# Kernel tuning notes

Measured on AMD Instinct MI355X. Metric: run time of the kernel, lower is better.

## Reference

```python
import math
import jax, jax.numpy as jnp
import numpy as np

N, E = 20000, 640000
S_DIM, Z_DIM, H, QK, VD = 64, 64, 4, 8, 8
EPS = 1e-8


def quat_rotate(v, q):
    # v: [..., 3], q: [..., 4] (w, x, y, z), broadcastable. Unit-quaternion rotation:
    # v' = v + 2*(w*(u x v) + u x (u x v))
    w = q[..., 0:1]
    u = q[..., 1:4]
    uv = jnp.cross(u, v)
    return v + 2.0 * (w * uv + jnp.cross(u, uv))


def setup_inputs() -> dict:
    key = jax.random.key(0)
    ks = jax.random.split(key, 16)
    s = jax.random.normal(ks[0], (N, S_DIM), dtype=jnp.float32)
    z = jax.random.normal(ks[1], (E, Z_DIM), dtype=jnp.float32)
    edge_index = jax.random.randint(ks[2], (2, E), 0, N)
    quaternion = jax.random.normal(ks[3], (N, 4), dtype=jnp.float32)
    quaternion = quaternion / jnp.linalg.norm(quaternion, axis=-1, keepdims=True)
    translation = jax.random.normal(ks[4], (N, 3), dtype=jnp.float32)
    sc_s = 1.0 / math.sqrt(S_DIM)
    sc_z = 1.0 / math.sqrt(Z_DIM)
    # weights stored [in, out] so y = x @ W (equivalent to torch x @ W.T)
    Wq_s = jax.random.normal(ks[5], (S_DIM, H * S_DIM), dtype=jnp.float32) * sc_s
    Wk_s = jax.random.normal(ks[6], (S_DIM, H * S_DIM), dtype=jnp.float32) * sc_s
    Wv_s = jax.random.normal(ks[7], (S_DIM, H * S_DIM), dtype=jnp.float32) * sc_s
    Wq_v = jax.random.normal(ks[8], (S_DIM, H * QK * 3), dtype=jnp.float32) * sc_s
    Wk_v = jax.random.normal(ks[9], (S_DIM, H * QK * 3), dtype=jnp.float32) * sc_s
    Wv_v = jax.random.normal(ks[10], (S_DIM, H * VD * 3), dtype=jnp.float32) * sc_s
    Wb = jax.random.normal(ks[11], (Z_DIM, H), dtype=jnp.float32) * sc_z
    bb = jnp.zeros((H,), dtype=jnp.float32)
    Wdz = jax.random.normal(ks[12], (Z_DIM, Z_DIM // 4), dtype=jnp.float32) * sc_z
    bdz = jnp.zeros((Z_DIM // 4,), dtype=jnp.float32)
    head_weights = jnp.full((H,), 0.541324854612918, dtype=jnp.float32)  # softplus^{-1}(1)
    concat_dim = Z_DIM // 4 + S_DIM + VD * 4
    Wout = jax.random.normal(ks[13], (H * concat_dim, S_DIM), dtype=jnp.float32) / math.sqrt(H * concat_dim)
    bout = jnp.zeros((S_DIM,), dtype=jnp.float32)
    return {
        's': s, 'z': z, 'edge_index': edge_index, 'quaternion': quaternion,
        'translation': translation, 'Wq_s': Wq_s, 'Wk_s': Wk_s, 'Wv_s': Wv_s,
        'Wq_v': Wq_v, 'Wk_v': Wk_v, 'Wv_v': Wv_v, 'Wb': Wb, 'bb': bb,
        'Wdz': Wdz, 'bdz': bdz, 'head_weights': head_weights,
        'Wout': Wout, 'bout': bout,
    }


def reference(s, z, edge_index, quaternion, translation,
              Wq_s, Wk_s, Wv_s, Wq_v, Wk_v, Wv_v,
              Wb, bb, Wdz, bdz, head_weights, Wout, bout):
    idx_i, idx_j = edge_index[0], edge_index[1]
    n = s.shape[0]
    h = head_weights.shape[0]
    qk = Wq_v.shape[1] // (3 * h)
    vd = Wv_v.shape[1] // (3 * h)

    q_scalar = (s @ Wq_s).reshape(n, h, -1)
    k_scalar = (s @ Wk_s).reshape(n, h, -1)
    v_scalar = (s @ Wv_s).reshape(n, h, -1)

    def to_points(x):
        # torch.split into 3 chunks then stack(dim=-1): [n, 3*c] -> [n, c, 3]
        c = x.shape[-1] // 3
        return jnp.swapaxes(x.reshape(n, 3, c), 1, 2)

    quat_b = quaternion[:, None, :]
    trans_b = translation[:, None, :]
    q_vec = (quat_rotate(to_points(s @ Wq_v), quat_b) + trans_b).reshape(n, h, qk, 3)
    k_vec = (quat_rotate(to_points(s @ Wk_v), quat_b) + trans_b).reshape(n, h, qk, 3)
    v_vec = (quat_rotate(to_points(s @ Wv_v), quat_b) + trans_b).reshape(n, h, vd, 3)

    b_bias = z @ Wb + bb  # [E, H]

    attn = jnp.sum(k_scalar[idx_i] * q_scalar[idx_j], axis=-1)  # [E, H]
    attn = attn * math.sqrt(1.0 / 3 * qk) + math.sqrt(1.0 / 3) * b_bias

    disp = q_vec[idx_i] - k_vec[idx_j]            # [E, H, qk, 3]
    vec_att = jnp.sum(disp * disp, axis=-1)       # [E, H, qk]
    hw = jax.nn.softplus(head_weights)[None, :, None]
    vec_att = jnp.sum(vec_att * hw, axis=-1) * math.sqrt(1.0 / (3 * (qk * 9.0 / 2))) * (-0.5)
    attn = attn + vec_att

    # segment softmax over destination node idx_i
    seg_max = jax.ops.segment_max(attn, idx_i, num_segments=n)
    ea = jnp.exp(attn - seg_max[idx_i])
    denom = jax.ops.segment_sum(ea, idx_i, num_segments=n)
    attn = ea / denom[idx_i]                      # [E, H]

    out_scalar = jax.ops.segment_sum(attn[:, :, None] * v_scalar[idx_i], idx_i, num_segments=n)
    out_scalar = out_scalar.reshape(n, -1)

    out_vec = jax.ops.segment_sum(attn[:, :, None, None] * v_vec[idx_i], idx_i, num_segments=n)
    out_vec = out_vec - translation[:, None, None, :]
    q_conj = jnp.concatenate([quaternion[:, :1], -quaternion[:, 1:]], axis=-1)
    out_vec = quat_rotate(out_vec, q_conj[:, None, None, :])   # [n, h, vd, 3]
    out_vec_norm = jnp.sqrt(jnp.sum(out_vec * out_vec, axis=-1) + EPS).reshape(n, -1)
    out_vec_flat = out_vec.reshape(n, -1, 3)

    pair_z = z @ Wdz + bdz                         # [E, z/4]
    out_pair = jax.ops.segment_sum(attn[:, :, None] * pair_z[:, None, :], idx_i, num_segments=n)
    out_pair = out_pair.reshape(n, -1)

    feats = jnp.concatenate([out_scalar,
                             out_vec_flat[..., 0], out_vec_flat[..., 1], out_vec_flat[..., 2],
                             out_vec_norm, out_pair], axis=-1)
    return feats @ Wout + bout
```

## Files before the change

### kernel.cpp

```cpp
#include <hip/hip_runtime.h>
#include <stdint.h>


#define C_SQRT83  1.6329931618554518f
#define C_SQRT13  0.5773502691896258f
#define C_VEC    -0.04811252243246881f

__device__ __forceinline__ unsigned short f2bf(float f){
  unsigned u = __float_as_uint(f);
  u += 0x7fffu + ((u >> 16) & 1u);
  return (unsigned short)(u >> 16);
}
__device__ __forceinline__ unsigned pack2(float a, float b){
  return (unsigned)f2bf(a) | ((unsigned)f2bf(b) << 16);
}
__device__ __forceinline__ float bflo(unsigned u){ return __uint_as_float(u << 16); }
__device__ __forceinline__ float bfhi(unsigned u){ return __uint_as_float(u & 0xffff0000u); }

__device__ __forceinline__ void quat_rot(float w, float ux, float uy, float uz,
                                         float vx, float vy, float vz,
                                         float& ox, float& oy, float& oz){
  float cx = uy*vz - uz*vy;
  float cy = uz*vx - ux*vz;
  float cz = ux*vy - uy*vx;
  float dx = uy*cz - uz*cy;
  float dy = uz*cx - ux*cz;
  float dz = ux*cy - uy*cx;
  ox = vx + 2.f*(w*cx + dx);
  oy = vy + 2.f*(w*cy + dy);
  oz = vz + 2.f*(w*cz + dz);
}


__global__ __launch_bounds__(256) void k_count(const int* __restrict__ ei,
                                               unsigned* __restrict__ counts,
                                               unsigned* __restrict__ rank, int ne){
  int e = blockIdx.x*256 + threadIdx.x;
  if (e >= ne) return;
  rank[e] = atomicAdd(&counts[ei[e]], 1u);
}

__global__ __launch_bounds__(256) void k_scan(const unsigned* __restrict__ counts,
                                              unsigned* __restrict__ row_off, int n){
  __shared__ unsigned part[256];
  int t = threadIdx.x;
  int chunk = (n + 255) >> 8;
  int s0 = t*chunk, s1 = min(s0 + chunk, n);
  unsigned sum = 0;
  for (int k = s0; k < s1; ++k) sum += counts[k];
  part[t] = sum; __syncthreads();
  for (int off = 1; off < 256; off <<= 1){
    unsigned v = (t >= off) ? part[t-off] : 0u;
    __syncthreads();
    part[t] += v;
    __syncthreads();
  }
  unsigned run = (t == 0) ? 0u : part[t-1];
  for (int k = s0; k < s1; ++k){
    row_off[k] = run; run += counts[k];
  }
  if (t == 255) row_off[n] = part[255];
}


#define BN 32

__device__ __forceinline__ void pass256(const float* __restrict__ W,
                                        const float stT[64][40], int cg, int sl,
                                        float acc[8][4]){
  #pragma unroll
  for (int i=0;i<8;i++){ acc[i][0]=0.f; acc[i][1]=0.f; acc[i][2]=0.f; acc[i][3]=0.f; }
  #pragma unroll 4
  for (int k = 0; k < 64; ++k){
    const float4 w  = *(const float4*)(W + (size_t)k*256 + cg*4);
    const float4 n0 = *(const float4*)&stT[k][sl*8];
    const float4 n1 = *(const float4*)&stT[k][sl*8+4];
    acc[0][0]+=n0.x*w.x; acc[0][1]+=n0.x*w.y; acc[0][2]+=n0.x*w.z; acc[0][3]+=n0.x*w.w;
    acc[1][0]+=n0.y*w.x; acc[1][1]+=n0.y*w.y; acc[1][2]+=n0.y*w.z; acc[1][3]+=n0.y*w.w;
    acc[2][0]+=n0.z*w.x; acc[2][1]+=n0.z*w.y; acc[2][2]+=n0.z*w.z; acc[2][3]+=n0.z*w.w;
    acc[3][0]+=n0.w*w.x; acc[3][1]+=n0.w*w.y; acc[3][2]+=n0.w*w.z; acc[3][3]+=n0.w*w.w;
    acc[4][0]+=n1.x*w.x; acc[4][1]+=n1.x*w.y; acc[4][2]+=n1.x*w.z; acc[4][3]+=n1.x*w.w;
    acc[5][0]+=n1.y*w.x; acc[5][1]+=n1.y*w.y; acc[5][2]+=n1.y*w.z; acc[5][3]+=n1.y*w.w;
    acc[6][0]+=n1.z*w.x; acc[6][1]+=n1.z*w.y; acc[6][2]+=n1.z*w.z; acc[6][3]+=n1.z*w.w;
    acc[7][0]+=n1.w*w.x; acc[7][1]+=n1.w*w.y; acc[7][2]+=n1.w*w.z; acc[7][3]+=n1.w*w.w;
  }
}

__device__ __forceinline__ void pass96(const float* __restrict__ W,
                                       const float stT[64][40], int cgp, int slp,
                                       float acc[4][4]){
  #pragma unroll
  for (int i=0;i<4;i++){ acc[i][0]=0.f; acc[i][1]=0.f; acc[i][2]=0.f; acc[i][3]=0.f; }
  if (cgp >= 24) return;
  #pragma unroll 4
  for (int k = 0; k < 64; ++k){
    const float4 w = *(const float4*)(W + (size_t)k*96 + cgp*4);
    const float4 nv = *(const float4*)&stT[k][slp*4];
    acc[0][0]+=nv.x*w.x; acc[0][1]+=nv.x*w.y; acc[0][2]+=nv.x*w.z; acc[0][3]+=nv.x*w.w;
    acc[1][0]+=nv.y*w.x; acc[1][1]+=nv.y*w.y; acc[1][2]+=nv.y*w.z; acc[1][3]+=nv.y*w.w;
    acc[2][0]+=nv.z*w.x; acc[2][1]+=nv.z*w.y; acc[2][2]+=nv.z*w.z; acc[2][3]+=nv.z*w.w;
    acc[3][0]+=nv.w*w.x; acc[3][1]+=nv.w*w.y; acc[3][2]+=nv.w*w.z; acc[3][3]+=nv.w*w.w;
  }
}

__global__ __launch_bounds__(256) void k_proj(
    const float* __restrict__ s, const float* __restrict__ quat, const float* __restrict__ trans,
    const float* __restrict__ Wqs, const float* __restrict__ Wks, const float* __restrict__ Wvs,
    const float* __restrict__ Wqv, const float* __restrict__ Wkv, const float* __restrict__ Wvv,
    unsigned* __restrict__ qs, unsigned* __restrict__ ks, float* __restrict__ vs,
    unsigned* __restrict__ qv, unsigned* __restrict__ kv, float* __restrict__ vv, int n)
{
  __shared__ float stT[64][40];
  __shared__ float pt[BN][97];
  const int tid = threadIdx.x;
  const int node0 = blockIdx.x * BN;

  #pragma unroll
  for (int r = 0; r < 2; ++r){
    const int idx = tid + r*256;
    const int nd = idx >> 4, c4 = idx & 15;
    const int g = node0 + nd;
    float4 v = make_float4(0.f,0.f,0.f,0.f);
    if (g < n) v = *(const float4*)(s + (size_t)g*64 + c4*4);
    stT[c4*4+0][nd]=v.x; stT[c4*4+1][nd]=v.y; stT[c4*4+2][nd]=v.z; stT[c4*4+3][nd]=v.w;
  }
  __syncthreads();

  const int cg = tid & 63, sl = tid >> 6;
  const int cgp = tid & 31, slp = tid >> 5;
  float acc[8][4];

  pass256(Wqs, stT, cg, sl, acc);
  #pragma unroll
  for (int i=0;i<8;i++){
    const int g = node0 + sl*8 + i;
    if (g < n){
      uint2 u; u.x = pack2(acc[i][0],acc[i][1]); u.y = pack2(acc[i][2],acc[i][3]);
      *(uint2*)(qs + (size_t)g*128 + cg*2) = u;
    }
  }
  pass256(Wks, stT, cg, sl, acc);
  #pragma unroll
  for (int i=0;i<8;i++){
    const int g = node0 + sl*8 + i;
    if (g < n){
      uint2 u; u.x = pack2(acc[i][0],acc[i][1]); u.y = pack2(acc[i][2],acc[i][3]);
      *(uint2*)(ks + (size_t)g*128 + cg*2) = u;
    }
  }
  pass256(Wvs, stT, cg, sl, acc);
  #pragma unroll
  for (int i=0;i<8;i++){
    const int g = node0 + sl*8 + i;
    if (g < n){
      float4 f; f.x=acc[i][0]; f.y=acc[i][1]; f.z=acc[i][2]; f.w=acc[i][3];
      *(float4*)(vs + (size_t)g*256 + cg*4) = f;
    }
  }

  float pac[4][4];

  pass96(Wqv, stT, cgp, slp, pac);
  __syncthreads();
  if (cgp < 24){
    #pragma unroll
    for (int i=0;i<4;i++){
      #pragma unroll
      for (int c=0;c<4;c++) pt[slp*4+i][cgp*4+c] = pac[i][c];
    }
  }
  __syncthreads();
  #pragma unroll
  for (int r = 0; r < 2; ++r){
    const int t2 = tid + r*256;
    const int nd = t2 >> 4, pp = t2 & 15;
    const int g = node0 + nd;
    if (g < n){
      const float4 q4 = *(const float4*)(quat + (size_t)g*4);
      const float tx = trans[(size_t)g*3], ty = trans[(size_t)g*3+1], tz = trans[(size_t)g*3+2];
      float x0,y0,z0,x1,y1,z1;
      quat_rot(q4.x,q4.y,q4.z,q4.w, pt[nd][2*pp],   pt[nd][32+2*pp],   pt[nd][64+2*pp],   x0,y0,z0);
      quat_rot(q4.x,q4.y,q4.z,q4.w, pt[nd][2*pp+1], pt[nd][32+2*pp+1], pt[nd][64+2*pp+1], x1,y1,z1);
      x0+=tx; y0+=ty; z0+=tz; x1+=tx; y1+=ty; z1+=tz;
      unsigned* d = qv + (size_t)g*48 + pp*3;
      d[0] = pack2(x0,y0); d[1] = pack2(z0,x1); d[2] = pack2(y1,z1);
    }
  }

  pass96(Wkv, stT, cgp, slp, pac);
  __syncthreads();
  if (cgp < 24){
    #pragma unroll
    for (int i=0;i<4;i++){
      #pragma unroll
      for (int c=0;c<4;c++) pt[slp*4+i][cgp*4+c] = pac[i][c];
    }
  }
  __syncthreads();
  #pragma unroll
  for (int r = 0; r < 2; ++r){
    const int t2 = tid + r*256;
    const int nd = t2 >> 4, pp = t2 & 15;
    const int g = node0 + nd;
    if (g < n){
      const float4 q4 = *(const float4*)(quat + (size_t)g*4);
      const float tx = trans[(size_t)g*3], ty = trans[(size_t)g*3+1], tz = trans[(size_t)g*3+2];
      float x0,y0,z0,x1,y1,z1;
      quat_rot(q4.x,q4.y,q4.z,q4.w, pt[nd][2*pp],   pt[nd][32+2*pp],   pt[nd][64+2*pp],   x0,y0,z0);
      quat_rot(q4.x,q4.y,q4.z,q4.w, pt[nd][2*pp+1], pt[nd][32+2*pp+1], pt[nd][64+2*pp+1], x1,y1,z1);
      x0+=tx; y0+=ty; z0+=tz; x1+=tx; y1+=ty; z1+=tz;
      unsigned* d = kv + (size_t)g*48 + pp*3;
      d[0] = pack2(x0,y0); d[1] = pack2(z0,x1); d[2] = pack2(y1,z1);
    }
  }

  pass96(Wvv, stT, cgp, slp, pac);
  __syncthreads();
  if (cgp < 24){
    #pragma unroll
    for (int i=0;i<4;i++){
      #pragma unroll
      for (int c=0;c<4;c++) pt[slp*4+i][cgp*4+c] = pac[i][c];
    }
  }
  __syncthreads();
  #pragma unroll
  for (int r = 0; r < 12; ++r){
    const int idx = tid + r*256;
    const int nd = idx / 96, col = idx - nd*96;
    const int g = node0 + nd;
    if (g < n) vv[(size_t)g*96 + col] = pt[nd][col];
  }
}


__global__ __launch_bounds__(256) void k_zf(
    const int* __restrict__ ei, const unsigned* __restrict__ rank,
    const unsigned* __restrict__ roff, const float* __restrict__ z,
    const float* __restrict__ Wb,  const float* __restrict__ bb,
    const float* __restrict__ Wdz, const float* __restrict__ bdz,
    unsigned* __restrict__ rec, int ne)
{
  __shared__ float zT[16][258];
  const int tid = threadIdx.x;
  const int E0  = blockIdx.x * 256;
  const int e   = E0 + tid;
  const bool full = (E0 + 256 <= ne);

  int i = 0, j = 0; unsigned pos = 0;
  if (e < ne){
    i = ei[e]; j = ei[ne + e];
    pos = roff[i] + rank[e];
  }

  float b4[4] = {0.f,0.f,0.f,0.f};
  float pacc[16];
  #pragma unroll
  for (int c=0;c<16;c++) pacc[c]=0.f;

  if (full){
    #pragma unroll
    for (int c = 0; c < 4; ++c){
      if (c) __syncthreads();
      #pragma unroll
      for (int q = 0; q < 4; ++q){
        const int idx = tid + q*256;
        const int row = idx >> 2, f4 = idx & 3;
        const float4 v = *(const float4*)(z + (size_t)(E0+row)*64 + c*16 + f4*4);
        zT[f4*4+0][row]=v.x; zT[f4*4+1][row]=v.y;
        zT[f4*4+2][row]=v.z; zT[f4*4+3][row]=v.w;
      }
      __syncthreads();
      const int kb = c*16;
      #pragma unroll
      for (int kk = 0; kk < 16; ++kk){
        const float zk = zT[kk][tid];
        const int k = kb + kk;
        const float4 wb = *(const float4*)(Wb + k*4);
        b4[0]+=zk*wb.x; b4[1]+=zk*wb.y; b4[2]+=zk*wb.z; b4[3]+=zk*wb.w;
        const float* wd = Wdz + k*16;
        const float4 w0=*(const float4*)(wd),   w1=*(const float4*)(wd+4),
                     w2=*(const float4*)(wd+8), w3=*(const float4*)(wd+12);
        pacc[ 0]+=zk*w0.x; pacc[ 1]+=zk*w0.y; pacc[ 2]+=zk*w0.z; pacc[ 3]+=zk*w0.w;
        pacc[ 4]+=zk*w1.x; pacc[ 5]+=zk*w1.y; pacc[ 6]+=zk*w1.z; pacc[ 7]+=zk*w1.w;
        pacc[ 8]+=zk*w2.x; pacc[ 9]+=zk*w2.y; pacc[10]+=zk*w2.z; pacc[11]+=zk*w2.w;
        pacc[12]+=zk*w3.x; pacc[13]+=zk*w3.y; pacc[14]+=zk*w3.z; pacc[15]+=zk*w3.w;
      }
    }
  } else if (e < ne){
    const float* zr = z + (size_t)e*64;
    for (int k4 = 0; k4 < 16; ++k4){
      const float4 zv = *(const float4*)(zr + 4*k4);
      #pragma unroll
      for (int kk = 0; kk < 4; ++kk){
        const int k = 4*k4 + kk;
        const float zk = (kk==0)?zv.x:((kk==1)?zv.y:((kk==2)?zv.z:zv.w));
        const float4 wb = *(const float4*)(Wb + k*4);
        b4[0]+=zk*wb.x; b4[1]+=zk*wb.y; b4[2]+=zk*wb.z; b4[3]+=zk*wb.w;
        const float* wd = Wdz + k*16;
        const float4 w0=*(const float4*)(wd),   w1=*(const float4*)(wd+4),
                     w2=*(const float4*)(wd+8), w3=*(const float4*)(wd+12);
        pacc[ 0]+=zk*w0.x; pacc[ 1]+=zk*w0.y; pacc[ 2]+=zk*w0.z; pacc[ 3]+=zk*w0.w;
        pacc[ 4]+=zk*w1.x; pacc[ 5]+=zk*w1.y; pacc[ 6]+=zk*w1.z; pacc[ 7]+=zk*w1.w;
        pacc[ 8]+=zk*w2.x; pacc[ 9]+=zk*w2.y; pacc[10]+=zk*w2.z; pacc[11]+=zk*w2.w;
        pacc[12]+=zk*w3.x; pacc[13]+=zk*w3.y; pacc[14]+=zk*w3.z; pacc[15]+=zk*w3.w;
      }
    }
  }

  if (e < ne){
    #pragma unroll
    for (int c=0;c<16;c++) pacc[c] += bdz[c];
    uint4 u0, u1;
    u0.x=pack2(pacc[0],pacc[1]);   u0.y=pack2(pacc[2],pacc[3]);
    u0.z=pack2(pacc[4],pacc[5]);   u0.w=pack2(pacc[6],pacc[7]);
    u1.x=pack2(pacc[8],pacc[9]);   u1.y=pack2(pacc[10],pacc[11]);
    u1.z=pack2(pacc[12],pacc[13]); u1.w=pack2(pacc[14],pacc[15]);
    float4 bo;
    bo.x = C_SQRT13*(b4[0] + bb[0]);
    bo.y = C_SQRT13*(b4[1] + bb[1]);
    bo.z = C_SQRT13*(b4[2] + bb[2]);
    bo.w = C_SQRT13*(b4[3] + bb[3]);
    uint4* d = (uint4*)rec + (size_t)pos*4;
    d[0] = *(uint4*)&bo;
    d[1] = u0;
    d[2] = u1;
    d[3] = make_uint4((unsigned)i, (unsigned)j, 0u, 0u);
  }
}


__global__ __launch_bounds__(256) void k_edge(
    const float* __restrict__ hwts,
    const unsigned* __restrict__ qs, const unsigned* __restrict__ ks,
    const unsigned* __restrict__ qv, const unsigned* __restrict__ kv,
    unsigned* __restrict__ rec, int ne)
{
  const int tid = threadIdx.x;
  const int P0  = blockIdx.x * 256;
  const int p   = P0 + tid;
  const bool full = (P0 + 256 <= ne);

  const float hw0 = C_VEC * log1pf(__expf(hwts[0]));
  const float hw1 = C_VEC * log1pf(__expf(hwts[1]));
  const float hw2 = C_VEC * log1pf(__expf(hwts[2]));
  const float hw3 = C_VEC * log1pf(__expf(hwts[3]));

  int i = 0, j = 0;
  float4 bias = make_float4(0.f,0.f,0.f,0.f);
  if (p < ne){
    bias = *(const float4*)((const float*)rec + (size_t)p*16);
    const uint2 ij = *(const uint2*)(rec + (size_t)p*16 + 12);
    i = (int)ij.x; j = (int)ij.y;
  }

  if (full){
    const int l = tid & 63;
    const int c = l & 3, g = l >> 2;
    #pragma unroll
    for (int sb = 0; sb < 4; ++sb){
      const int el = sb*16 + g;
      const int ie = __shfl(i, el, 64);
      const int je = __shfl(j, el, 64);

      const uint4* kr = (const uint4*)ks + (size_t)ie*32;
      const uint4* qr = (const uint4*)qs + (size_t)je*32;
      float s0=0.f, s1=0.f, s2=0.f, s3=0.f;
      #pragma unroll
      for (int it = 0; it < 8; ++it){
        const uint4 a = kr[it*4 + c];
        const uint4 b = qr[it*4 + c];
        float d;
        d  = bflo(a.x)*bflo(b.x) + bfhi(a.x)*bfhi(b.x);
        d += bflo(a.y)*bflo(b.y) + bfhi(a.y)*bfhi(b.y);
        d += bflo(a.z)*bflo(b.z) + bfhi(a.z)*bfhi(b.z);
        d += bflo(a.w)*bflo(b.w) + bfhi(a.w)*bfhi(b.w);
        if      (it < 2) s0 += d;
        else if (it < 4) s1 += d;
        else if (it < 6) s2 += d;
        else             s3 += d;
      }

      const uint4* qvr = (const uint4*)qv + (size_t)ie*12;
      const uint4* kvr = (const uint4*)kv + (size_t)je*12;
      float v0=0.f, v1=0.f, v2=0.f, v3=0.f;
      {
        const uint4 a = qvr[c], b = kvr[c];
        float d, t;
        t = bflo(a.x)-bflo(b.x); d  = t*t;  t = bfhi(a.x)-bfhi(b.x); d += t*t;
        t = bflo(a.y)-bflo(b.y); d += t*t;  t = bfhi(a.y)-bfhi(b.y); d += t*t;
        t = bflo(a.z)-bflo(b.z); d += t*t;  t = bfhi(a.z)-bfhi(b.z); d += t*t;
        t = bflo(a.w)-bflo(b.w); d += t*t;  t = bfhi(a.w)-bfhi(b.w); d += t*t;
        if (c < 3) v0 += d; else v1 += d;
      }
      {
        const uint4 a = qvr[4+c], b = kvr[4+c];
        float d, t;
        t = bflo(a.x)-bflo(b.x); d  = t*t;  t = bfhi(a.x)-bfhi(b.x); d += t*t;
        t = bflo(a.y)-bflo(b.y); d += t*t;  t = bfhi(a.y)-bfhi(b.y); d += t*t;
        t = bflo(a.z)-bflo(b.z); d += t*t;  t = bfhi(a.z)-bfhi(b.z); d += t*t;
        t = bflo(a.w)-bflo(b.w); d += t*t;  t = bfhi(a.w)-bfhi(b.w); d += t*t;
        if (c < 2) v1 += d; else v2 += d;
      }
      {
        const uint4 a = qvr[8+c], b = kvr[8+c];
        float d, t;
        t = bflo(a.x)-bflo(b.x); d  = t*t;  t = bfhi(a.x)-bfhi(b.x); d += t*t;
        t = bflo(a.y)-bflo(b.y); d += t*t;  t = bfhi(a.y)-bfhi(b.y); d += t*t;
        t = bflo(a.z)-bflo(b.z); d += t*t;  t = bfhi(a.z)-bfhi(b.z); d += t*t;
        t = bflo(a.w)-bflo(b.w); d += t*t;  t = bfhi(a.w)-bfhi(b.w); d += t*t;
        if (c < 1) v2 += d; else v3 += d;
      }

      float p0 = C_SQRT83*s0 + hw0*v0;
      float p1 = C_SQRT83*s1 + hw1*v1;
      float p2 = C_SQRT83*s2 + hw2*v2;
      float p3 = C_SQRT83*s3 + hw3*v3;
      #pragma unroll
      for (int msk = 1; msk < 4; msk <<= 1){
        p0 += __shfl_xor(p0, msk, 64);
        p1 += __shfl_xor(p1, msk, 64);
        p2 += __shfl_xor(p2, msk, 64);
        p3 += __shfl_xor(p3, msk, 64);
      }
      const float pc = (c==0)?p0:((c==1)?p1:((c==2)?p2:p3));

      const int srcbase = (l & 15) << 2;
      const float q0 = __shfl(pc, srcbase+0, 64);
      const float q1 = __shfl(pc, srcbase+1, 64);
      const float q2 = __shfl(pc, srcbase+2, 64);
      const float q3 = __shfl(pc, srcbase+3, 64);
      if ((l >> 4) == sb){
        float4 lg; lg.x = q0 + bias.x; lg.y = q1 + bias.y;
        lg.z = q2 + bias.z; lg.w = q3 + bias.w;
        *((uint4*)rec + (size_t)p*4) = *(uint4*)&lg;
      }
    }
  } else if (p < ne){
    const uint4* kr = (const uint4*)ks + (size_t)i*32;
    const uint4* qr = (const uint4*)qs + (size_t)j*32;
    float sdot[4];
    #pragma unroll
    for (int h = 0; h < 4; ++h){
      float acc = 0.f;
      #pragma unroll
      for (int cc = 0; cc < 8; ++cc){
        const uint4 a = kr[h*8+cc];
        const uint4 b = qr[h*8+cc];
        acc += bflo(a.x)*bflo(b.x) + bfhi(a.x)*bfhi(b.x);
        acc += bflo(a.y)*bflo(b.y) + bfhi(a.y)*bfhi(b.y);
        acc += bflo(a.z)*bflo(b.z) + bfhi(a.z)*bfhi(b.z);
        acc += bflo(a.w)*bflo(b.w) + bfhi(a.w)*bfhi(b.w);
      }
      sdot[h] = acc;
    }
    const uint4* qvr = (const uint4*)qv + (size_t)i*12;
    const uint4* kvr = (const uint4*)kv + (size_t)j*12;
    float vsum[4];
    #pragma unroll
    for (int h = 0; h < 4; ++h){
      float acc = 0.f;
      #pragma unroll
      for (int cc = 0; cc < 3; ++cc){
        const uint4 a = qvr[h*3+cc];
        const uint4 b = kvr[h*3+cc];
        float d;
        d = bflo(a.x)-bflo(b.x); acc += d*d;  d = bfhi(a.x)-bfhi(b.x); acc += d*d;
        d = bflo(a.y)-bflo(b.y); acc += d*d;  d = bfhi(a.y)-bfhi(b.y); acc += d*d;
        d = bflo(a.z)-bflo(b.z); acc += d*d;  d = bfhi(a.z)-bfhi(b.z); acc += d*d;
        d = bflo(a.w)-bflo(b.w); acc += d*d;  d = bfhi(a.w)-bfhi(b.w); acc += d*d;
      }
      vsum[h] = acc;
    }
    float4 lg;
    lg.x = C_SQRT83*sdot[0] + bias.x + hw0*vsum[0];
    lg.y = C_SQRT83*sdot[1] + bias.y + hw1*vsum[1];
    lg.z = C_SQRT83*sdot[2] + bias.z + hw2*vsum[2];
    lg.w = C_SQRT83*sdot[3] + bias.w + hw3*vsum[3];
    *((uint4*)rec + (size_t)p*4) = *(uint4*)&lg;
  }
}


__global__ __launch_bounds__(256) void k_soft(
    const unsigned* __restrict__ rec,
    const unsigned* __restrict__ row_off, float* __restrict__ out_pair, int n)
{
  const int node = blockIdx.x*4 + (threadIdx.x >> 6);
  if (node >= n) return;
  const int lane = threadIdx.x & 63;
  const int beg = (int)row_off[node], end = (int)row_off[node+1];
  const float* recf = (const float*)rec;

  float m[4] = {-3.0e38f,-3.0e38f,-3.0e38f,-3.0e38f};
  for (int p = beg + lane; p < end; p += 64){
    const float4 l = *(const float4*)(recf + (size_t)p*16);
    m[0]=fmaxf(m[0],l.x); m[1]=fmaxf(m[1],l.y); m[2]=fmaxf(m[2],l.z); m[3]=fmaxf(m[3],l.w);
  }
  #pragma unroll
  for (int msk = 1; msk < 64; msk <<= 1){
    #pragma unroll
    for (int h=0;h<4;h++) m[h] = fmaxf(m[h], __shfl_xor(m[h], msk));
  }
  float S[4] = {0.f,0.f,0.f,0.f};
  for (int p = beg + lane; p < end; p += 64){
    const float4 l = *(const float4*)(recf + (size_t)p*16);
    S[0]+=__expf(l.x-m[0]); S[1]+=__expf(l.y-m[1]);
    S[2]+=__expf(l.z-m[2]); S[3]+=__expf(l.w-m[3]);
  }
  #pragma unroll
  for (int msk = 1; msk < 64; msk <<= 1){
    #pragma unroll
    for (int h=0;h<4;h++) S[h] += __shfl_xor(S[h], msk);
  }
  float inv[4];
  #pragma unroll
  for (int h=0;h<4;h++) inv[h] = (S[h] > 0.f) ? (1.f/S[h]) : 0.f;

  const int e4 = lane >> 4, c = lane & 15;
  float acc[4] = {0.f,0.f,0.f,0.f};
  for (int base = beg; base < end; base += 4){
    const int p = base + e4;
    if (p < end){
      const float4 l = *(const float4*)(recf + (size_t)p*16);
      const unsigned u = rec[(size_t)p*16 + 4 + (c>>1)];
      const float pzv = (c & 1) ? bfhi(u) : bflo(u);
      acc[0] += __expf(l.x-m[0]) * pzv;
      acc[1] += __expf(l.y-m[1]) * pzv;
      acc[2] += __expf(l.z-m[2]) * pzv;
      acc[3] += __expf(l.w-m[3]) * pzv;
    }
  }
  #pragma unroll
  for (int msk = 16; msk < 64; msk <<= 1){
    #pragma unroll
    for (int h=0;h<4;h++) acc[h] += __shfl_xor(acc[h], msk);
  }
  const int hOut = lane >> 4;
  out_pair[(size_t)node*64 + lane] = acc[hOut] * inv[hOut];
}


__global__ __launch_bounds__(256) void k_out(
    const float* __restrict__ vs, const float* __restrict__ vv,
    const float* __restrict__ out_pair, const unsigned* __restrict__ row_off,
    const float* __restrict__ quat, const float* __restrict__ trans,
    const float* __restrict__ Wout, const float* __restrict__ bout,
    float* __restrict__ out, int n)
{
  __shared__ float feats[32][448];
  __shared__ int degs[32];
  const int tid = threadIdx.x;
  const int node0 = blockIdx.x*32;

  if (tid < 32){
    const int g = node0 + tid;
    degs[tid] = (g < n) ? (int)(row_off[g+1] - row_off[g]) : 1;
  }
  __syncthreads();

  for (int x = tid; x < 32*256; x += 256){
    const int nd = x >> 8, c = x & 255;
    const int g = node0 + nd;
    feats[nd][c] = (g < n && degs[nd] > 0) ? vs[(size_t)g*256 + c] : 0.f;
  }
  for (int x = tid; x < 32*64; x += 256){
    const int nd = x >> 6, c = x & 63;
    const int g = node0 + nd;
    feats[nd][384 + c] = (g < n) ? out_pair[(size_t)g*64 + c] : 0.f;
  }
  for (int x = tid; x < 32*32; x += 256){
    const int nd = x >> 5, pt = x & 31;
    const int g = node0 + nd;
    float X=0.f, Y=0.f, Z=0.f;
    if (g < n){
      if (degs[nd] > 0){
        X = vv[(size_t)g*96 + pt];
        Y = vv[(size_t)g*96 + 32 + pt];
        Z = vv[(size_t)g*96 + 64 + pt];
      } else {
        const float4 q4 = *(const float4*)(quat + (size_t)g*4);
        const float tx = trans[(size_t)g*3], ty = trans[(size_t)g*3+1], tz = trans[(size_t)g*3+2];
        quat_rot(q4.x, -q4.y, -q4.z, -q4.w, -tx, -ty, -tz, X, Y, Z);
      }
    }
    feats[nd][256 + pt] = X;
    feats[nd][288 + pt] = Y;
    feats[nd][320 + pt] = Z;
    feats[nd][352 + pt] = sqrtf(X*X + Y*Y + Z*Z + 1e-8f);
  }
  __syncthreads();

  const int lane = tid & 63;
  const int wave = tid >> 6;
  float acc[8];
  #pragma unroll
  for (int q8=0;q8<8;q8++) acc[q8]=0.f;

  for (int k0 = 0; k0 < 448; k0 += 4){
    const float w0 = Wout[(size_t)(k0+0)*64 + lane];
    const float w1 = Wout[(size_t)(k0+1)*64 + lane];
    const float w2 = Wout[(size_t)(k0+2)*64 + lane];
    const float w3 = Wout[(size_t)(k0+3)*64 + lane];
    #pragma unroll
    for (int q8 = 0; q8 < 8; ++q8){
      const float4 f = *(const float4*)&feats[wave*8 + q8][k0];
      acc[q8] += f.x*w0 + f.y*w1 + f.z*w2 + f.w*w3;
    }
  }
  const float bo = bout[lane];
  #pragma unroll
  for (int q8 = 0; q8 < 8; ++q8){
    const int g = node0 + wave*8 + q8;
    if (g < n) out[(size_t)g*64 + lane] = acc[q8] + bo;
  }
}


extern "C" void kernel_launch(void* const* d_in, const int* in_sizes, int n_in,
                              void* d_out, int out_size, void* d_ws, size_t ws_size,
                              hipStream_t stream) {
  const float* s     = (const float*)d_in[0];
  const float* z     = (const float*)d_in[1];
  const int*   ei    = (const int*)  d_in[2];
  const float* quat  = (const float*)d_in[3];
  const float* trans = (const float*)d_in[4];
  const float* Wqs   = (const float*)d_in[5];
  const float* Wks   = (const float*)d_in[6];
  const float* Wvs   = (const float*)d_in[7];
  const float* Wqv   = (const float*)d_in[8];
  const float* Wkv   = (const float*)d_in[9];
  const float* Wvv   = (const float*)d_in[10];
  const float* Wb    = (const float*)d_in[11];
  const float* bb    = (const float*)d_in[12];
  const float* Wdz   = (const float*)d_in[13];
  const float* bdz   = (const float*)d_in[14];
  const float* hwts  = (const float*)d_in[15];
  const float* Wout  = (const float*)d_in[16];
  const float* bout  = (const float*)d_in[17];
  float* out = (float*)d_out;

  const int n  = in_sizes[0] / 64;
  const int ne = in_sizes[1] / 64;

  size_t off = 0;
  char* base = (char*)d_ws;
  auto take = [&](size_t bytes)->char* {
    char* p = base + off;
    off += (bytes + 255) & ~(size_t)255;
    return p;
  };
  unsigned* qs     = (unsigned*)take((size_t)n*512);
  unsigned* ks     = (unsigned*)take((size_t)n*512);
  unsigned* qvt    = (unsigned*)take((size_t)n*192);
  unsigned* kvt    = (unsigned*)take((size_t)n*192);
  float*    vs     = (float*)   take((size_t)n*1024);
  float*    vv     = (float*)   take((size_t)n*384);
  unsigned* rec    = (unsigned*)take((size_t)ne*64);
  unsigned* counts = (unsigned*)take((size_t)n*4);
  unsigned* roff   = (unsigned*)take((size_t)(n+1)*4);
  unsigned* rank   = (unsigned*)take((size_t)ne*4);
  float*    opair  = (float*)   take((size_t)n*256);
  (void)ws_size; (void)n_in; (void)out_size;

  const int gbE = (ne + 255) / 256;

  hipMemsetAsync(counts, 0, (size_t)n*4, stream);
  k_count<<<gbE, 256, 0, stream>>>(ei, counts, rank, ne);
  k_scan <<<1,   256, 0, stream>>>(counts, roff, n);
  k_proj <<<(n + BN - 1)/BN, 256, 0, stream>>>(s, quat, trans, Wqs, Wks, Wvs, Wqv, Wkv, Wvv,
                                               qs, ks, vs, qvt, kvt, vv, n);
  k_zf   <<<gbE, 256, 0, stream>>>(ei, rank, roff, z, Wb, bb, Wdz, bdz, rec, ne);
  k_edge <<<gbE, 256, 0, stream>>>(hwts, qs, ks, qvt, kvt, rec, ne);
  k_soft <<<(n + 3)/4, 256, 0, stream>>>(rec, roff, opair, n);
  k_out  <<<(n + 31)/32, 256, 0, stream>>>(vs, vv, opair, roff, quat, trans,
                                           Wout, bout, out, n);
}
```

Baseline: 598.3 us.

## Split edge logits into separate array, prefetch z tiles, shrink output node tile

Moves the per-edge logits/bias out of the 64-byte edge record into a compact 16-byte-per-edge array. The softmax max/sum passes and the edge kernel then read dense float4s instead of strided records. The z-projection kernel now double-buffers its global loads in registers, so the next chunk loads while the current chunk computes. The output projection kernel uses 16 nodes per block instead of 32, which cuts shared memory and raises block count but gives less Wout reuse per block.

```diff
diff --git a/kernel.cpp b/kernel.cpp
--- a/kernel.cpp
+++ b/kernel.cpp
@@ -239,7 +239,7 @@
     const unsigned* __restrict__ roff, const float* __restrict__ z,
     const float* __restrict__ Wb,  const float* __restrict__ bb,
     const float* __restrict__ Wdz, const float* __restrict__ bdz,
-    unsigned* __restrict__ rec, int ne)
+    float* __restrict__ lg, unsigned* __restrict__ rec, int ne)
 {
   __shared__ float zT[16][258];
   const int tid = threadIdx.x;
@@ -259,18 +259,33 @@
   for (int c=0;c<16;c++) pacc[c]=0.f;
 
   if (full){
+    float4 rg[4];
+    #pragma unroll
+    for (int q = 0; q < 4; ++q){
+      const int idx = tid + q*256;
+      const int row = idx >> 2, f4 = idx & 3;
+      rg[q] = *(const float4*)(z + (size_t)(E0+row)*64 + f4*4);
+    }
+    #pragma unroll
+    for (int q = 0; q < 4; ++q){
+      const int idx = tid + q*256;
+      const int row = idx >> 2, f4 = idx & 3;
+      zT[f4*4+0][row]=rg[q].x; zT[f4*4+1][row]=rg[q].y;
+      zT[f4*4+2][row]=rg[q].z; zT[f4*4+3][row]=rg[q].w;
+    }
+    __syncthreads();
+
     #pragma unroll
     for (int c = 0; c < 4; ++c){
-      if (c) __syncthreads();
-      #pragma unroll
-      for (int q = 0; q < 4; ++q){
-        const int idx = tid + q*256;
-        const int row = idx >> 2, f4 = idx & 3;
-        const float4 v = *(const float4*)(z + (size_t)(E0+row)*64 + c*16 + f4*4);
-        zT[f4*4+0][row]=v.x; zT[f4*4+1][row]=v.y;
-        zT[f4*4+2][row]=v.z; zT[f4*4+3][row]=v.w;
-      }
-      __syncthreads();
+      float4 rn[4];
+      if (c < 3){
+        #pragma unroll
+        for (int q = 0; q < 4; ++q){
+          const int idx = tid + q*256;
+          const int row = idx >> 2, f4 = idx & 3;
+          rn[q] = *(const float4*)(z + (size_t)(E0+row)*64 + (c+1)*16 + f4*4);
+        }
+      }
       const int kb = c*16;
       #pragma unroll
       for (int kk = 0; kk < 16; ++kk){
@@ -286,6 +301,17 @@
         pacc[ 8]+=zk*w2.x; pacc[ 9]+=zk*w2.y; pacc[10]+=zk*w2.z; pacc[11]+=zk*w2.w;
         pacc[12]+=zk*w3.x; pacc[13]+=zk*w3.y; pacc[14]+=zk*w3.z; pacc[15]+=zk*w3.w;
       }
+      __syncthreads();
+      if (c < 3){
+        #pragma unroll
+        for (int q = 0; q < 4; ++q){
+          const int idx = tid + q*256;
+          const int row = idx >> 2, f4 = idx & 3;
+          zT[f4*4+0][row]=rn[q].x; zT[f4*4+1][row]=rn[q].y;
+          zT[f4*4+2][row]=rn[q].z; zT[f4*4+3][row]=rn[q].w;
+        }
+        __syncthreads();
+      }
     }
   } else if (e < ne){
     const float* zr = z + (size_t)e*64;
@@ -321,11 +347,11 @@
     bo.y = C_SQRT13*(b4[1] + bb[1]);
     bo.z = C_SQRT13*(b4[2] + bb[2]);
     bo.w = C_SQRT13*(b4[3] + bb[3]);
+    *((float4*)lg + pos) = bo;
     uint4* d = (uint4*)rec + (size_t)pos*4;
-    d[0] = *(uint4*)&bo;
-    d[1] = u0;
-    d[2] = u1;
-    d[3] = make_uint4((unsigned)i, (unsigned)j, 0u, 0u);
+    d[0] = u0;
+    d[1] = u1;
+    d[2] = make_uint4((unsigned)i, (unsigned)j, 0u, 0u);
   }
 }
 
@@ -334,7 +360,7 @@
     const float* __restrict__ hwts,
     const unsigned* __restrict__ qs, const unsigned* __restrict__ ks,
     const unsigned* __restrict__ qv, const unsigned* __restrict__ kv,
-    unsigned* __restrict__ rec, int ne)
+    const unsigned* __restrict__ rec, float* __restrict__ lg, int ne)
 {
   const int tid = threadIdx.x;
   const int P0  = blockIdx.x * 256;
@@ -349,8 +375,8 @@
   int i = 0, j = 0;
   float4 bias = make_float4(0.f,0.f,0.f,0.f);
   if (p < ne){
-    bias = *(const float4*)((const float*)rec + (size_t)p*16);
-    const uint2 ij = *(const uint2*)(rec + (size_t)p*16 + 12);
+    bias = *((const float4*)lg + p);
+    const uint2 ij = *(const uint2*)(rec + (size_t)p*16 + 8);
     i = (int)ij.x; j = (int)ij.y;
   }
 
@@ -431,9 +457,9 @@
       const float q2 = __shfl(pc, srcbase+2, 64);
       const float q3 = __shfl(pc, srcbase+3, 64);
       if ((l >> 4) == sb){
-        float4 lg; lg.x = q0 + bias.x; lg.y = q1 + bias.y;
-        lg.z = q2 + bias.z; lg.w = q3 + bias.w;
-        *((uint4*)rec + (size_t)p*4) = *(uint4*)&lg;
+        float4 lgv; lgv.x = q0 + bias.x; lgv.y = q1 + bias.y;
+        lgv.z = q2 + bias.z; lgv.w = q3 + bias.w;
+        *((float4*)lg + p) = lgv;
       }
     }
   } else if (p < ne){
@@ -472,29 +498,29 @@
       }
       vsum[h] = acc;
     }
-    float4 lg;
-    lg.x = C_SQRT83*sdot[0] + bias.x + hw0*vsum[0];
-    lg.y = C_SQRT83*sdot[1] + bias.y + hw1*vsum[1];
-    lg.z = C_SQRT83*sdot[2] + bias.z + hw2*vsum[2];
-    lg.w = C_SQRT83*sdot[3] + bias.w + hw3*vsum[3];
-    *((uint4*)rec + (size_t)p*4) = *(uint4*)&lg;
+    float4 lgv;
+    lgv.x = C_SQRT83*sdot[0] + bias.x + hw0*vsum[0];
+    lgv.y = C_SQRT83*sdot[1] + bias.y + hw1*vsum[1];
+    lgv.z = C_SQRT83*sdot[2] + bias.z + hw2*vsum[2];
+    lgv.w = C_SQRT83*sdot[3] + bias.w + hw3*vsum[3];
+    *((float4*)lg + p) = lgv;
   }
 }
 
 
 __global__ __launch_bounds__(256) void k_soft(
-    const unsigned* __restrict__ rec,
+    const float* __restrict__ lg, const unsigned* __restrict__ rec,
     const unsigned* __restrict__ row_off, float* __restrict__ out_pair, int n)
 {
   const int node = blockIdx.x*4 + (threadIdx.x >> 6);
   if (node >= n) return;
   const int lane = threadIdx.x & 63;
   const int beg = (int)row_off[node], end = (int)row_off[node+1];
-  const float* recf = (const float*)rec;
+  const float4* lg4 = (const float4*)lg;
 
   float m[4] = {-3.0e38f,-3.0e38f,-3.0e38f,-3.0e38f};
   for (int p = beg + lane; p < end; p += 64){
-    const float4 l = *(const float4*)(recf + (size_t)p*16);
+    const float4 l = lg4[p];
     m[0]=fmaxf(m[0],l.x); m[1]=fmaxf(m[1],l.y); m[2]=fmaxf(m[2],l.z); m[3]=fmaxf(m[3],l.w);
   }
   #pragma unroll
@@ -504,7 +530,7 @@
   }
   float S[4] = {0.f,0.f,0.f,0.f};
   for (int p = beg + lane; p < end; p += 64){
-    const float4 l = *(const float4*)(recf + (size_t)p*16);
+    const float4 l = lg4[p];
     S[0]+=__expf(l.x-m[0]); S[1]+=__expf(l.y-m[1]);
     S[2]+=__expf(l.z-m[2]); S[3]+=__expf(l.w-m[3]);
   }
@@ -522,8 +548,8 @@
   for (int base = beg; base < end; base += 4){
     const int p = base + e4;
     if (p < end){
-      const float4 l = *(const float4*)(recf + (size_t)p*16);
-      const unsigned u = rec[(size_t)p*16 + 4 + (c>>1)];
+      const float4 l = lg4[p];
+      const unsigned u = rec[(size_t)p*16 + (c>>1)];
       const float pzv = (c & 1) ? bfhi(u) : bflo(u);
       acc[0] += __expf(l.x-m[0]) * pzv;
       acc[1] += __expf(l.y-m[1]) * pzv;
@@ -540,6 +566,8 @@
   out_pair[(size_t)node*64 + lane] = acc[hOut] * inv[hOut];
 }
 
+
+#define BNO 16
 
 __global__ __launch_bounds__(256) void k_out(
     const float* __restrict__ vs, const float* __restrict__ vv,
@@ -548,28 +576,28 @@
     const float* __restrict__ Wout, const float* __restrict__ bout,
     float* __restrict__ out, int n)
 {
-  __shared__ float feats[32][448];
-  __shared__ int degs[32];
+  __shared__ float feats[BNO][448];
+  __shared__ int degs[BNO];
   const int tid = threadIdx.x;
-  const int node0 = blockIdx.x*32;
-
-  if (tid < 32){
+  const int node0 = blockIdx.x*BNO;
+
+  if (tid < BNO){
     const int g = node0 + tid;
     degs[tid] = (g < n) ? (int)(row_off[g+1] - row_off[g]) : 1;
   }
   __syncthreads();
 
-  for (int x = tid; x < 32*256; x += 256){
+  for (int x = tid; x < BNO*256; x += 256){
     const int nd = x >> 8, c = x & 255;
     const int g = node0 + nd;
     feats[nd][c] = (g < n && degs[nd] > 0) ? vs[(size_t)g*256 + c] : 0.f;
   }
-  for (int x = tid; x < 32*64; x += 256){
+  for (int x = tid; x < BNO*64; x += 256){
     const int nd = x >> 6, c = x & 63;
     const int g = node0 + nd;
     feats[nd][384 + c] = (g < n) ? out_pair[(size_t)g*64 + c] : 0.f;
   }
-  for (int x = tid; x < 32*32; x += 256){
+  for (int x = tid; x < BNO*32; x += 256){
     const int nd = x >> 5, pt = x & 31;
     const int g = node0 + nd;
     float X=0.f, Y=0.f, Z=0.f;
@@ -593,9 +621,9 @@
 
   const int lane = tid & 63;
   const int wave = tid >> 6;
-  float acc[8];
-  #pragma unroll
-  for (int q8=0;q8<8;q8++) acc[q8]=0.f;
+  float acc[4];
+  #pragma unroll
+  for (int q4=0;q4<4;q4++) acc[q4]=0.f;
 
   for (int k0 = 0; k0 < 448; k0 += 4){
     const float w0 = Wout[(size_t)(k0+0)*64 + lane];
@@ -603,16 +631,16 @@
     const float w2 = Wout[(size_t)(k0+2)*64 + lane];
     const float w3 = Wout[(size_t)(k0+3)*64 + lane];
     #pragma unroll
-    for (int q8 = 0; q8 < 8; ++q8){
-      const float4 f = *(const float4*)&feats[wave*8 + q8][k0];
-      acc[q8] += f.x*w0 + f.y*w1 + f.z*w2 + f.w*w3;
+    for (int q4 = 0; q4 < 4; ++q4){
+      const float4 f = *(const float4*)&feats[wave*4 + q4][k0];
+      acc[q4] += f.x*w0 + f.y*w1 + f.z*w2 + f.w*w3;
     }
   }
   const float bo = bout[lane];
   #pragma unroll
-  for (int q8 = 0; q8 < 8; ++q8){
-    const int g = node0 + wave*8 + q8;
-    if (g < n) out[(size_t)g*64 + lane] = acc[q8] + bo;
+  for (int q4 = 0; q4 < 4; ++q4){
+    const int g = node0 + wave*4 + q4;
+    if (g < n) out[(size_t)g*64 + lane] = acc[q4] + bo;
   }
 }
 
@@ -656,6 +684,7 @@
   unsigned* kvt    = (unsigned*)take((size_t)n*192);
   float*    vs     = (float*)   take((size_t)n*1024);
   float*    vv     = (float*)   take((size_t)n*384);
+  float*    lg     = (float*)   take((size_t)ne*16);
   unsigned* rec    = (unsigned*)take((size_t)ne*64);
   unsigned* counts = (unsigned*)take((size_t)n*4);
   unsigned* roff   = (unsigned*)take((size_t)(n+1)*4);
@@ -670,9 +699,9 @@
   k_scan <<<1,   256, 0, stream>>>(counts, roff, n);
   k_proj <<<(n + BN - 1)/BN, 256, 0, stream>>>(s, quat, trans, Wqs, Wks, Wvs, Wqv, Wkv, Wvv,
                                                qs, ks, vs, qvt, kvt, vv, n);
-  k_zf   <<<gbE, 256, 0, stream>>>(ei, rank, roff, z, Wb, bb, Wdz, bdz, rec, ne);
-  k_edge <<<gbE, 256, 0, stream>>>(hwts, qs, ks, qvt, kvt, rec, ne);
-  k_soft <<<(n + 3)/4, 256, 0, stream>>>(rec, roff, opair, n);
-  k_out  <<<(n + 31)/32, 256, 0, stream>>>(vs, vv, opair, roff, quat, trans,
-                                           Wout, bout, out, n);
-}
+  k_zf   <<<gbE, 256, 0, stream>>>(ei, rank, roff, z, Wb, bb, Wdz, bdz, lg, rec, ne);
+  k_edge <<<gbE, 256, 0, stream>>>(hwts, qs, ks, qvt, kvt, rec, lg, ne);
+  k_soft <<<(n + 3)/4, 256, 0, stream>>>(lg, rec, roff, opair, n);
+  k_out  <<<(n + BNO - 1)/BNO, 256, 0, stream>>>(vs, vv, opair, roff, quat, trans,
+                                                 Wout, bout, out, n);
+}
```

Measured after the change: 591.0 us. Within noise of the previous version (-1.2%).
